# Kernel tuning notes

Measured on AMD Instinct MI355X. Metric: run time of the kernel, lower is better.

## Reference

```python
import jax, jax.numpy as jnp
import numpy as np


def _lstm_layer(x, Wih, Whh, bih, bhh):
    # x: [M, T, D]; Wih: [4H, D]; Whh: [4H, H]; torch gate order i, f, g, o
    M, T, D = x.shape
    H = Whh.shape[1]
    xg = jnp.einsum('mtd,gd->mtg', x, Wih) + bih + bhh  # [M, T, 4H]

    def step(carry, xg_t):
        h, c = carry
        g = xg_t + h @ Whh.T
        i, f, gg, o = jnp.split(g, 4, axis=-1)
        c = jax.nn.sigmoid(f) * c + jax.nn.sigmoid(i) * jnp.tanh(gg)
        h = jax.nn.sigmoid(o) * jnp.tanh(c)
        return (h, c), h

    h0 = jnp.zeros((M, H), x.dtype)
    (_, _), hs = jax.lax.scan(step, (h0, h0), jnp.swapaxes(xg, 0, 1))
    return jnp.swapaxes(hs, 0, 1)  # [M, T, H]


def setup_inputs() -> dict:
    key = jax.random.key(0)
    ks = jax.random.split(key, 16)
    B, T, N = 16, 64, 512
    GH, LH, OUT = 64, 64, 1
    s = 0.1
    inp = {
        'X': jax.random.normal(ks[0], (B, T, N), jnp.float32),
        'adj': jax.random.uniform(ks[1], (N, N), jnp.float32),
        'gcn1_W': jax.random.normal(ks[2], (GH, 1), jnp.float32) * s,
        'gcn1_b': jax.random.normal(ks[3], (GH,), jnp.float32) * s,
        'gcn2_W': jax.random.normal(ks[4], (GH, GH), jnp.float32) * s,
        'gcn2_b': jax.random.normal(ks[5], (GH,), jnp.float32) * s,
        'Wih0': jax.random.normal(ks[6], (4 * LH, GH), jnp.float32) * s,
        'Whh0': jax.random.normal(ks[7], (4 * LH, LH), jnp.float32) * s,
        'bih0': jax.random.normal(ks[8], (4 * LH,), jnp.float32) * s,
        'bhh0': jax.random.normal(ks[9], (4 * LH,), jnp.float32) * s,
        'Wih1': jax.random.normal(ks[10], (4 * LH, LH), jnp.float32) * s,
        'Whh1': jax.random.normal(ks[11], (4 * LH, LH), jnp.float32) * s,
        'bih1': jax.random.normal(ks[12], (4 * LH,), jnp.float32) * s,
        'bhh1': jax.random.normal(ks[13], (4 * LH,), jnp.float32) * s,
        'fc_W': jax.random.normal(ks[14], (OUT, LH), jnp.float32) * s,
        'fc_b': jax.random.normal(ks[15], (OUT,), jnp.float32) * s,
    }
    return inp


def reference(X, adj, gcn1_W, gcn1_b, gcn2_W, gcn2_b,
              Wih0, Whh0, bih0, bhh0, Wih1, Whh1, bih1, bhh1,
              fc_W, fc_b):
    B, T, N = X.shape
    x = X[..., None]  # [B, T, N, 1]
    # GCN layer 1: bmm(A, X) then linear + relu, vectorized over all timesteps
    h = jnp.einsum('nm,btmd->btnd', adj, x)
    h = jax.nn.relu(jnp.einsum('btnd,gd->btng', h, gcn1_W) + gcn1_b)
    # GCN layer 2
    h = jnp.einsum('nm,btmg->btng', adj, h)
    h = jax.nn.relu(jnp.einsum('btng,hg->btnh', h, gcn2_W) + gcn2_b)
    # Per-node LSTM == one batched LSTM over B*N sequences (shared weights)
    GH = h.shape[-1]
    seqs = jnp.transpose(h, (0, 2, 1, 3)).reshape(B * N, T, GH)  # [B*N, T, GH]
    y = _lstm_layer(seqs, Wih0, Whh0, bih0, bhh0)
    y = _lstm_layer(y, Wih1, Whh1, bih1, bhh1)
    last = y[:, -1, :].reshape(B, N, -1)  # [B, N, LH]
    out = jnp.einsum('bnh,oh->bno', last, fc_W) + fc_b  # [B, N, 1]
    return out
```

## Files before the change

### kernel.cpp

```cpp
#include <hip/hip_runtime.h>
#include <hip/hip_bf16.h>

#define Bb 16
#define Tt 64
#define Nn 512
#define BT (Bb*Tt)
#define LH 64
#define Mseq (Bb*Nn)

typedef short  bf16x8 __attribute__((ext_vector_type(8)));
typedef float  f32x16 __attribute__((ext_vector_type(16)));

__device__ __forceinline__ unsigned short f2bf(float f) {
    unsigned int u = __float_as_uint(f);
    return (unsigned short)((u + 0x7FFFu + ((u >> 16) & 1u)) >> 16);
}
__device__ __forceinline__ float bf2f(unsigned short b) {
    return __uint_as_float(((unsigned int)b) << 16);
}
__device__ __forceinline__ void split8(const float* v, bf16x8& hi, bf16x8& lo) {
#pragma unroll
    for (int i = 0; i < 8; ++i) {
        unsigned short h = f2bf(v[i]);
        hi[i] = (short)h;
        lo[i] = (short)f2bf(v[i] - bf2f(h));
    }
}
__device__ __forceinline__ float sigf(float x)  { return 1.f / (1.f + __expf(-x)); }
__device__ __forceinline__ float tanhfast(float x) { return 2.f / (1.f + __expf(-2.f * x)) - 1.f; }

__global__ __launch_bounds__(256) void sgemm_kernel(
    const float* __restrict__ X, const float* __restrict__ adj,
    float* __restrict__ S)
{
    __shared__ __align__(16) float Xs[64 * 68];
    __shared__ __align__(16) float As[64 * 68];
    const int tid = threadIdx.x;
    const int nb  = blockIdx.x * 64;
    const int bt0 = blockIdx.y * 64;

    const int lr  = tid >> 4;
    const int lc4 = (tid & 15) * 4;
    const int r0  = 4 * (tid >> 4);
    const int c0  = 4 * (tid & 15);

    float acc[4][4] = {};

    for (int kc = 0; kc < 8; ++kc) {
        __syncthreads();
#pragma unroll
        for (int s = 0; s < 64; s += 16) {
            *(float4*)&Xs[(lr + s) * 68 + lc4] =
                *(const float4*)&X[(size_t)(bt0 + lr + s) * Nn + kc * 64 + lc4];
            *(float4*)&As[(lr + s) * 68 + lc4] =
                *(const float4*)&adj[(size_t)(nb + lr + s) * Nn + kc * 64 + lc4];
        }
        __syncthreads();
#pragma unroll 4
        for (int k4 = 0; k4 < 64; k4 += 4) {
            float4 x4[4], a4[4];
#pragma unroll
            for (int i = 0; i < 4; ++i) x4[i] = *(float4*)&Xs[(r0 + i) * 68 + k4];
#pragma unroll
            for (int j = 0; j < 4; ++j) a4[j] = *(float4*)&As[(c0 + j) * 68 + k4];
#pragma unroll
            for (int i = 0; i < 4; ++i)
#pragma unroll
                for (int j = 0; j < 4; ++j)
                    acc[i][j] += x4[i].x * a4[j].x + x4[i].y * a4[j].y +
                                 x4[i].z * a4[j].z + x4[i].w * a4[j].w;
        }
    }
#pragma unroll
    for (int i = 0; i < 4; ++i) {
        float4 v = make_float4(acc[i][0], acc[i][1], acc[i][2], acc[i][3]);
        *(float4*)&S[(size_t)(bt0 + r0 + i) * Nn + nb + c0] = v;
    }
}

__global__ __launch_bounds__(256) void adjpack_kernel(
    const float* __restrict__ adj, short* __restrict__ Phi, short* __restrict__ Plo)
{
    const int id   = blockIdx.x * 256 + threadIdx.x;
    const int lane = id & 63;
    const int ks   = (id >> 6) & 3;
    const int sub  = (id >> 8) & 1;
    const int mc   = (id >> 9) & 7;
    const int nt   = (id >> 12) & 7;
    const int row  = nt * 64 + sub * 32 + (lane & 31);

    float v[8];
#pragma unroll
    for (int e = 0; e < 8; ++e) {
        int kk = ((lane >> 5) << 3) + e;
        int ml = ((ks >> 1) << 5) + (kk & 3) + ((kk >> 2) << 3) + ((ks & 1) << 2);
        v[e] = adj[(size_t)row * Nn + mc * 64 + ml];
    }
    bf16x8 hi, lo;
    split8(v, hi, lo);
    *(bf16x8*)&Phi[(size_t)id * 8] = hi;
    *(bf16x8*)&Plo[(size_t)id * 8] = lo;
}

__global__ __launch_bounds__(256) void gcnz_kernel(
    const float* __restrict__ S,
    const short* __restrict__ Phi, const short* __restrict__ Plo,
    const float* __restrict__ w1g, const float* __restrict__ b1g,
    const float* __restrict__ W2, const float* __restrict__ b2g,
    unsigned* __restrict__ outbuf)
{
    __shared__ __align__(16) short zhi[16384];
    __shared__ __align__(16) short zlo[16384];

    const int tid = threadIdx.x;
    const int l   = tid & 63;
    const int w   = tid >> 6;
    const int l31 = l & 31;
    const int lh  = l >> 5;
    const int bt  = blockIdx.x >> 1;
    const int hh  = blockIdx.x & 1;

    bf16x8 w2H[4], w2L[4];
#pragma unroll
    for (int ks = 0; ks < 4; ++ks) {
        int g0 = ks * 16 + lh * 8;
        float v[8];
        *(float4*)&v[0] = *(const float4*)&W2[(size_t)(hh * 32 + l31) * 64 + g0];
        *(float4*)&v[4] = *(const float4*)&W2[(size_t)(hh * 32 + l31) * 64 + g0 + 4];
        split8(v, w2H[ks], w2L[ks]);
    }

#pragma unroll
    for (int mcp = 0; mcp < 2; ++mcp) {
        const int mc = w * 2 + mcp;
#pragma unroll
        for (int msub = 0; msub < 2; ++msub) {
            float s = S[(size_t)bt * Nn + mc * 64 + msub * 32 + l31];
            f32x16 a;
#pragma unroll
            for (int r = 0; r < 16; ++r) a[r] = 0.f;
#pragma unroll
            for (int ks = 0; ks < 4; ++ks) {
                int g0 = ks * 16 + lh * 8;
                float4 wa = *(const float4*)&w1g[g0];
                float4 wb = *(const float4*)&w1g[g0 + 4];
                float4 ba = *(const float4*)&b1g[g0];
                float4 bb = *(const float4*)&b1g[g0 + 4];
                float hv[8];
                hv[0] = fmaxf(s * wa.x + ba.x, 0.f); hv[1] = fmaxf(s * wa.y + ba.y, 0.f);
                hv[2] = fmaxf(s * wa.z + ba.z, 0.f); hv[3] = fmaxf(s * wa.w + ba.w, 0.f);
                hv[4] = fmaxf(s * wb.x + bb.x, 0.f); hv[5] = fmaxf(s * wb.y + bb.y, 0.f);
                hv[6] = fmaxf(s * wb.z + bb.z, 0.f); hv[7] = fmaxf(s * wb.w + bb.w, 0.f);
                bf16x8 h1h, h1l;
                split8(hv, h1h, h1l);
                a = __builtin_amdgcn_mfma_f32_32x32x16_bf16(h1h, w2H[ks], a, 0, 0, 0);
                a = __builtin_amdgcn_mfma_f32_32x32x16_bf16(h1h, w2L[ks], a, 0, 0, 0);
                a = __builtin_amdgcn_mfma_f32_32x32x16_bf16(h1l, w2H[ks], a, 0, 0, 0);
            }
            const int ks_st = msub * 2 + lh;
#pragma unroll
            for (int half = 0; half < 2; ++half) {
                bf16x8 sh, sl;
#pragma unroll
                for (int e = 0; e < 8; ++e) {
                    float v = a[half * 8 + e];
                    unsigned short h = f2bf(v);
                    sh[e] = (short)h;
                    sl[e] = (short)f2bf(v - bf2f(h));
                }
                unsigned off = (unsigned)((mc * 4 + ks_st) * 1024 + (half * 32 + l31) * 16);
                *(bf16x8*)((char*)zhi + off) = sh;
                *(bf16x8*)((char*)zlo + off) = sl;
            }
        }
    }
    __syncthreads();

    const int b = bt >> 6, t = bt & 63;
    const float b2v = b2g[hh * 32 + l31];
#pragma unroll
    for (int nt2 = 0; nt2 < 2; ++nt2) {
        const int nt = w * 2 + nt2;
#pragma unroll
        for (int nsub = 0; nsub < 2; ++nsub) {
            f32x16 a;
#pragma unroll
            for (int r = 0; r < 16; ++r) a[r] = b2v;
            for (int mc = 0; mc < 8; ++mc) {
#pragma unroll
                for (int ks = 0; ks < 4; ++ks) {
                    size_t fo = ((((size_t)(nt * 8 + mc) * 2 + nsub) * 4 + ks) * 64 + l) * 8;
                    bf16x8 ah = *(const bf16x8*)&Phi[fo];
                    bf16x8 al = *(const bf16x8*)&Plo[fo];
                    unsigned zo = (unsigned)((mc * 4 + ks) * 1024 + l * 16);
                    bf16x8 bh = *(bf16x8*)((char*)zhi + zo);
                    bf16x8 bl = *(bf16x8*)((char*)zlo + zo);
                    a = __builtin_amdgcn_mfma_f32_32x32x16_bf16(ah, bh, a, 0, 0, 0);
                    a = __builtin_amdgcn_mfma_f32_32x32x16_bf16(ah, bl, a, 0, 0, 0);
                    a = __builtin_amdgcn_mfma_f32_32x32x16_bf16(al, bh, a, 0, 0, 0);
                }
            }
            const int h = hh * 32 + l31;
#pragma unroll
            for (int r = 0; r < 16; ++r) {
                int n = nt * 64 + nsub * 32 + (r & 3) + 8 * (r >> 2) + 4 * lh;
                float v = fmaxf(a[r], 0.f);
                unsigned short hb = f2bf(v);
                unsigned short lb = f2bf(v - bf2f(hb));
                outbuf[((size_t)(b * Nn + n) * Tt + t) * 64 + h] =
                    ((unsigned)hb << 16) | (unsigned)lb;
            }
        }
    }
}

#define FRS 1072
template <bool LAST>
__global__ __launch_bounds__(512) void lstm_kernel(
    const unsigned* __restrict__ xin, unsigned* __restrict__ yout,
    const float* __restrict__ Wih, const float* __restrict__ Whh,
    const float* __restrict__ bih, const float* __restrict__ bhh,
    const float* __restrict__ fcW, const float* __restrict__ fcb,
    float* __restrict__ out)
{
    __shared__ __align__(16) char xh_[4 * FRS];
    __shared__ __align__(16) char xl_[4 * FRS];
    __shared__ __align__(16) char hh_[4 * FRS];
    __shared__ __align__(16) char hl_[4 * FRS];
    __shared__ float fcp[32 * 17];

    const int tid = threadIdx.x;
    const int l   = tid & 63;
    const int w   = tid >> 6;
    const int l31 = l & 31;
    const int lh1 = l >> 5;
    const int s0  = blockIdx.x * 32;

    bf16x8 wiH[4], wiL[4], whH[4], whL[4];
    {
        const int jg = ((l31 >> 3) << 6) + w * 8 + (l31 & 7);
#pragma unroll
        for (int ks = 0; ks < 4; ++ks) {
            int k0 = ks * 16 + lh1 * 8;
            float v[8];
            *(float4*)&v[0] = *(const float4*)&Wih[(size_t)jg * 64 + k0];
            *(float4*)&v[4] = *(const float4*)&Wih[(size_t)jg * 64 + k0 + 4];
            split8(v, wiH[ks], wiL[ks]);
            *(float4*)&v[0] = *(const float4*)&Whh[(size_t)jg * 64 + k0];
            *(float4*)&v[4] = *(const float4*)&Whh[(size_t)jg * 64 + k0 + 4];
            split8(v, whH[ks], whL[ks]);
        }
    }
    float bias_r[16];
#pragma unroll
    for (int r = 0; r < 16; ++r) {
        int j = ((r >> 2) << 6) + w * 8 + (r & 3) + 4 * lh1;
        bias_r[r] = bih[j] + bhh[j];
    }
    float fw[4];
    if constexpr (LAST) {
#pragma unroll
        for (int i = 0; i < 4; ++i) fw[i] = fcW[w * 8 + 4 * lh1 + i];
    }

    for (int i = tid; i < 4 * FRS / 4; i += 512) {
        ((int*)hh_)[i] = 0;
        ((int*)hl_)[i] = 0;
    }

    const int sm = tid >> 4;
    const int sk = (tid & 15) * 4;
    const unsigned stb = (unsigned)((sk >> 4) * FRS + ((((sk >> 3) & 1) << 5) + sm) * 16 + (sk & 7) * 2);
    const unsigned hwb = (unsigned)((w >> 1) * FRS + (((w & 1) << 5) + l31) * 16 + lh1 * 8);

    float cst[4] = {0.f, 0.f, 0.f, 0.f};
    short4 hph = {0, 0, 0, 0}, hpl = {0, 0, 0, 0};
    float hfin[4];

    uint4 xp = *(const uint4*)&xin[((size_t)(s0 + sm) * Tt + 0) * 64 + sk];

    for (int t = 0; t < Tt; ++t) {
        short4 sh, sl;
        sh.x = (short)(xp.x >> 16); sl.x = (short)(xp.x & 0xffff);
        sh.y = (short)(xp.y >> 16); sl.y = (short)(xp.y & 0xffff);
        sh.z = (short)(xp.z >> 16); sl.z = (short)(xp.z & 0xffff);
        sh.w = (short)(xp.w >> 16); sl.w = (short)(xp.w & 0xffff);
        *(short4*)(xh_ + stb) = sh;
        *(short4*)(xl_ + stb) = sl;
        if (t > 0) {
            *(short4*)(hh_ + hwb) = hph;
            *(short4*)(hl_ + hwb) = hpl;
        }
        {
            int tn = (t < Tt - 1) ? t + 1 : t;
            xp = *(const uint4*)&xin[((size_t)(s0 + sm) * Tt + tn) * 64 + sk];
        }
        __syncthreads();

        f32x16 a1, a2;
#pragma unroll
        for (int r = 0; r < 16; ++r) { a1[r] = 0.f; a2[r] = 0.f; }
#pragma unroll
        for (int ks = 0; ks < 4; ++ks) {
            bf16x8 xh = *(bf16x8*)(xh_ + ks * FRS + l * 16);
            bf16x8 xl = *(bf16x8*)(xl_ + ks * FRS + l * 16);
            a1 = __builtin_amdgcn_mfma_f32_32x32x16_bf16(wiH[ks], xh, a1, 0, 0, 0);
            a1 = __builtin_amdgcn_mfma_f32_32x32x16_bf16(wiL[ks], xh, a1, 0, 0, 0);
            a1 = __builtin_amdgcn_mfma_f32_32x32x16_bf16(wiH[ks], xl, a1, 0, 0, 0);
            bf16x8 hh = *(bf16x8*)(hh_ + ks * FRS + l * 16);
            bf16x8 hl = *(bf16x8*)(hl_ + ks * FRS + l * 16);
            a2 = __builtin_amdgcn_mfma_f32_32x32x16_bf16(whH[ks], hh, a2, 0, 0, 0);
            a2 = __builtin_amdgcn_mfma_f32_32x32x16_bf16(whL[ks], hh, a2, 0, 0, 0);
            a2 = __builtin_amdgcn_mfma_f32_32x32x16_bf16(whH[ks], hl, a2, 0, 0, 0);
        }

        unsigned yq[4];
#pragma unroll
        for (int ui = 0; ui < 4; ++ui) {
            float gi = a1[ui]      + a2[ui]      + bias_r[ui];
            float gf = a1[4 + ui]  + a2[4 + ui]  + bias_r[4 + ui];
            float gg = a1[8 + ui]  + a2[8 + ui]  + bias_r[8 + ui];
            float go = a1[12 + ui] + a2[12 + ui] + bias_r[12 + ui];
            float c  = sigf(gf) * cst[ui] + sigf(gi) * tanhfast(gg);
            float hv = sigf(go) * tanhfast(c);
            cst[ui] = c;
            unsigned short hb = f2bf(hv);
            unsigned short lb = f2bf(hv - bf2f(hb));
            ((short*)&hph)[ui] = (short)hb;
            ((short*)&hpl)[ui] = (short)lb;
            if constexpr (!LAST) {
                yq[ui] = ((unsigned)hb << 16) | (unsigned)lb;
            } else {
                if (t == Tt - 1) hfin[ui] = hv;
            }
        }
        if constexpr (!LAST) {
            *(uint4*)&yout[((size_t)(s0 + l31) * Tt + t) * 64 + w * 8 + 4 * lh1] =
                make_uint4(yq[0], yq[1], yq[2], yq[3]);
        }
        __syncthreads();
    }

    if constexpr (LAST) {
        float part = hfin[0] * fw[0] + hfin[1] * fw[1] + hfin[2] * fw[2] + hfin[3] * fw[3];
        fcp[l31 * 17 + w * 2 + lh1] = part;
        __syncthreads();
        if (tid < 32) {
            float s = fcb[0];
#pragma unroll
            for (int i = 0; i < 16; ++i) s += fcp[tid * 17 + i];
            out[s0 + tid] = s;
        }
    }
}

extern "C" void kernel_launch(void* const* d_in, const int* in_sizes, int n_in,
                              void* d_out, int out_size, void* d_ws, size_t ws_size,
                              hipStream_t stream) {
    const float* X      = (const float*)d_in[0];
    const float* adj    = (const float*)d_in[1];
    const float* gcn1_W = (const float*)d_in[2];
    const float* gcn1_b = (const float*)d_in[3];
    const float* gcn2_W = (const float*)d_in[4];
    const float* gcn2_b = (const float*)d_in[5];
    const float* Wih0   = (const float*)d_in[6];
    const float* Whh0   = (const float*)d_in[7];
    const float* bih0   = (const float*)d_in[8];
    const float* bhh0   = (const float*)d_in[9];
    const float* Wih1   = (const float*)d_in[10];
    const float* Whh1   = (const float*)d_in[11];
    const float* bih1   = (const float*)d_in[12];
    const float* bhh1   = (const float*)d_in[13];
    const float* fc_W   = (const float*)d_in[14];
    const float* fc_b   = (const float*)d_in[15];

    char* base = (char*)d_ws;
    float*    S      = (float*)base;
    unsigned* buf0   = (unsigned*)(base + (size_t)BT * Nn * 4);
    short*    adjPhi = (short*)(base + (size_t)BT * Nn * 4 + (size_t)Mseq * Tt * LH * 4);
    short*    adjPlo = adjPhi + 32768 * 8;

    sgemm_kernel<<<dim3(Nn / 64, BT / 64), 256, 0, stream>>>(X, adj, S);
    adjpack_kernel<<<128, 256, 0, stream>>>(adj, adjPhi, adjPlo);
    gcnz_kernel<<<2048, 256, 0, stream>>>(
        S, adjPhi, adjPlo, gcn1_W, gcn1_b, gcn2_W, gcn2_b, buf0);
    lstm_kernel<false><<<Mseq / 32, 512, 0, stream>>>(
        buf0, buf0, Wih0, Whh0, bih0, bhh0, nullptr, nullptr, nullptr);
    lstm_kernel<true><<<Mseq / 32, 512, 0, stream>>>(
        buf0, nullptr, Wih1, Whh1, bih1, bhh1, fc_W, fc_b, (float*)d_out);
}
```

Before: 644.3 us.

## Fuse GCN layer-2 bmm with per-timestep weight matmul and split LSTM accumulators

The GCN kernel no longer stages the full Z=h1·W2 for a timestep in shared memory. Each block now handles four timesteps (one per wave) and one 64-node tile, computing Z chunks in registers and feeding them straight into the adjacency bmm, with the adjacency fragments repacked to match. This removes the 64KB LDS buffer and its barrier and adds an occupancy hint, but every wave now reloads adjacency fragments from global memory and recomputes the split-bf16 conversion. In the LSTM kernel, the MFMA chain uses two independent accumulator pairs to shorten dependency chains, and the x/h staging moves after the compute with an extra barrier.

```diff
diff --git a/kernel.cpp b/kernel.cpp
--- a/kernel.cpp
+++ b/kernel.cpp
@@ -81,142 +81,168 @@
 __global__ __launch_bounds__(256) void adjpack_kernel(
     const float* __restrict__ adj, short* __restrict__ Phi, short* __restrict__ Plo)
 {
-    const int id   = blockIdx.x * 256 + threadIdx.x;
-    const int lane = id & 63;
-    const int ks   = (id >> 6) & 3;
-    const int sub  = (id >> 8) & 1;
-    const int mc   = (id >> 9) & 7;
-    const int nt   = (id >> 12) & 7;
-    const int row  = nt * 64 + sub * 32 + (lane & 31);
+    const int g    = blockIdx.x * 256 + threadIdx.x;
+    const int lane = g & 63;
+    const int ks   = (g >> 6) & 1;
+    const int ns   = (g >> 7) & 1;
+    const int ms   = (g >> 8) & 15;
+    const int nt   = (g >> 12) & 7;
+    const int n    = nt * 64 + ns * 32 + (lane & 31);
+    const int lh   = lane >> 5;
 
     float v[8];
 #pragma unroll
     for (int e = 0; e < 8; ++e) {
-        int kk = ((lane >> 5) << 3) + e;
-        int ml = ((ks >> 1) << 5) + (kk & 3) + ((kk >> 2) << 3) + ((ks & 1) << 2);
-        v[e] = adj[(size_t)row * Nn + mc * 64 + ml];
+        int pi = ks * 16 + lh * 4 + (e & 3) + 8 * (e >> 2);
+        v[e] = adj[(size_t)n * Nn + ms * 32 + pi];
     }
     bf16x8 hi, lo;
     split8(v, hi, lo);
-    *(bf16x8*)&Phi[(size_t)id * 8] = hi;
-    *(bf16x8*)&Plo[(size_t)id * 8] = lo;
-}
-
-__global__ __launch_bounds__(256) void gcnz_kernel(
+    *(bf16x8*)&Phi[(size_t)g * 8] = hi;
+    *(bf16x8*)&Plo[(size_t)g * 8] = lo;
+}
+
+__device__ __forceinline__ void bmm_step(
+    const f32x16& az, const short* __restrict__ Phi, const short* __restrict__ Plo,
+    size_t abase, int l, f32x16& acc_ns0, f32x16& acc_ns1)
+{
+    bf16x8 zH[2], zL[2];
+#pragma unroll
+    for (int kb = 0; kb < 2; ++kb) {
+#pragma unroll
+        for (int e = 0; e < 8; ++e) {
+            float v = az[kb * 8 + e];
+            unsigned short hb = f2bf(v);
+            zH[kb][e] = (short)hb;
+            zL[kb][e] = (short)f2bf(v - bf2f(hb));
+        }
+    }
+#pragma unroll
+    for (int ns = 0; ns < 2; ++ns) {
+#pragma unroll
+        for (int kb = 0; kb < 2; ++kb) {
+            size_t fo = abase + (size_t)((ns * 2 + kb) * 64 + l) * 8;
+            bf16x8 ah = *(const bf16x8*)&Phi[fo];
+            bf16x8 al = *(const bf16x8*)&Plo[fo];
+            if (ns == 0) {
+                acc_ns0 = __builtin_amdgcn_mfma_f32_32x32x16_bf16(ah, zH[kb], acc_ns0, 0, 0, 0);
+                acc_ns0 = __builtin_amdgcn_mfma_f32_32x32x16_bf16(ah, zL[kb], acc_ns0, 0, 0, 0);
+                acc_ns0 = __builtin_amdgcn_mfma_f32_32x32x16_bf16(al, zH[kb], acc_ns0, 0, 0, 0);
+            } else {
+                acc_ns1 = __builtin_amdgcn_mfma_f32_32x32x16_bf16(ah, zH[kb], acc_ns1, 0, 0, 0);
+                acc_ns1 = __builtin_amdgcn_mfma_f32_32x32x16_bf16(ah, zL[kb], acc_ns1, 0, 0, 0);
+                acc_ns1 = __builtin_amdgcn_mfma_f32_32x32x16_bf16(al, zH[kb], acc_ns1, 0, 0, 0);
+            }
+        }
+    }
+}
+
+__global__ __launch_bounds__(256, 2) void gcnz_kernel(
     const float* __restrict__ S,
     const short* __restrict__ Phi, const short* __restrict__ Plo,
     const float* __restrict__ w1g, const float* __restrict__ b1g,
     const float* __restrict__ W2, const float* __restrict__ b2g,
     unsigned* __restrict__ outbuf)
 {
-    __shared__ __align__(16) short zhi[16384];
-    __shared__ __align__(16) short zlo[16384];
-
     const int tid = threadIdx.x;
     const int l   = tid & 63;
     const int w   = tid >> 6;
     const int l31 = l & 31;
     const int lh  = l >> 5;
-    const int bt  = blockIdx.x >> 1;
-    const int hh  = blockIdx.x & 1;
-
-    bf16x8 w2H[4], w2L[4];
-#pragma unroll
-    for (int ks = 0; ks < 4; ++ks) {
-        int g0 = ks * 16 + lh * 8;
-        float v[8];
-        *(float4*)&v[0] = *(const float4*)&W2[(size_t)(hh * 32 + l31) * 64 + g0];
-        *(float4*)&v[4] = *(const float4*)&W2[(size_t)(hh * 32 + l31) * 64 + g0 + 4];
-        split8(v, w2H[ks], w2L[ks]);
-    }
-
-#pragma unroll
-    for (int mcp = 0; mcp < 2; ++mcp) {
-        const int mc = w * 2 + mcp;
-#pragma unroll
-        for (int msub = 0; msub < 2; ++msub) {
-            float s = S[(size_t)bt * Nn + mc * 64 + msub * 32 + l31];
-            f32x16 a;
-#pragma unroll
-            for (int r = 0; r < 16; ++r) a[r] = 0.f;
-#pragma unroll
-            for (int ks = 0; ks < 4; ++ks) {
-                int g0 = ks * 16 + lh * 8;
+    const int btg = blockIdx.x >> 3;
+    const int nt  = blockIdx.x & 7;
+    const int bt  = btg * 4 + w;
+
+    bf16x8 w2H[2][4], w2L[2][4];
+#pragma unroll
+    for (int hh = 0; hh < 2; ++hh)
+#pragma unroll
+        for (int kg = 0; kg < 4; ++kg) {
+            float v[8];
+            const float* p = &W2[(size_t)(hh * 32 + l31) * 64 + kg * 16 + lh * 8];
+            *(float4*)&v[0] = *(const float4*)&p[0];
+            *(float4*)&v[4] = *(const float4*)&p[4];
+            split8(v, w2H[hh][kg], w2L[hh][kg]);
+        }
+
+    f32x16 o00, o01, o10, o11;
+    {
+        float b20 = b2g[l31], b21 = b2g[32 + l31];
+#pragma unroll
+        for (int r = 0; r < 16; ++r) { o00[r] = b20; o01[r] = b21; o10[r] = b20; o11[r] = b21; }
+    }
+
+    const float* Srow = &S[(size_t)bt * Nn];
+
+    for (int mc = 0; mc < 8; ++mc) {
+#pragma unroll
+        for (int ms = 0; ms < 2; ++ms) {
+            const float sv = Srow[mc * 64 + ms * 32 + l31];
+            f32x16 az0, az1;
+#pragma unroll
+            for (int r = 0; r < 16; ++r) { az0[r] = 0.f; az1[r] = 0.f; }
+#pragma unroll
+            for (int kg = 0; kg < 4; ++kg) {
+                int g0 = kg * 16 + lh * 8;
                 float4 wa = *(const float4*)&w1g[g0];
                 float4 wb = *(const float4*)&w1g[g0 + 4];
                 float4 ba = *(const float4*)&b1g[g0];
                 float4 bb = *(const float4*)&b1g[g0 + 4];
                 float hv[8];
-                hv[0] = fmaxf(s * wa.x + ba.x, 0.f); hv[1] = fmaxf(s * wa.y + ba.y, 0.f);
-                hv[2] = fmaxf(s * wa.z + ba.z, 0.f); hv[3] = fmaxf(s * wa.w + ba.w, 0.f);
-                hv[4] = fmaxf(s * wb.x + bb.x, 0.f); hv[5] = fmaxf(s * wb.y + bb.y, 0.f);
-                hv[6] = fmaxf(s * wb.z + bb.z, 0.f); hv[7] = fmaxf(s * wb.w + bb.w, 0.f);
+                hv[0] = fmaxf(sv * wa.x + ba.x, 0.f); hv[1] = fmaxf(sv * wa.y + ba.y, 0.f);
+                hv[2] = fmaxf(sv * wa.z + ba.z, 0.f); hv[3] = fmaxf(sv * wa.w + ba.w, 0.f);
+                hv[4] = fmaxf(sv * wb.x + bb.x, 0.f); hv[5] = fmaxf(sv * wb.y + bb.y, 0.f);
+                hv[6] = fmaxf(sv * wb.z + bb.z, 0.f); hv[7] = fmaxf(sv * wb.w + bb.w, 0.f);
                 bf16x8 h1h, h1l;
                 split8(hv, h1h, h1l);
-                a = __builtin_amdgcn_mfma_f32_32x32x16_bf16(h1h, w2H[ks], a, 0, 0, 0);
-                a = __builtin_amdgcn_mfma_f32_32x32x16_bf16(h1h, w2L[ks], a, 0, 0, 0);
-                a = __builtin_amdgcn_mfma_f32_32x32x16_bf16(h1l, w2H[ks], a, 0, 0, 0);
+                az0 = __builtin_amdgcn_mfma_f32_32x32x16_bf16(h1h, w2H[0][kg], az0, 0, 0, 0);
+                az0 = __builtin_amdgcn_mfma_f32_32x32x16_bf16(h1h, w2L[0][kg], az0, 0, 0, 0);
+                az0 = __builtin_amdgcn_mfma_f32_32x32x16_bf16(h1l, w2H[0][kg], az0, 0, 0, 0);
+                az1 = __builtin_amdgcn_mfma_f32_32x32x16_bf16(h1h, w2H[1][kg], az1, 0, 0, 0);
+                az1 = __builtin_amdgcn_mfma_f32_32x32x16_bf16(h1h, w2L[1][kg], az1, 0, 0, 0);
+                az1 = __builtin_amdgcn_mfma_f32_32x32x16_bf16(h1l, w2H[1][kg], az1, 0, 0, 0);
             }
-            const int ks_st = msub * 2 + lh;
-#pragma unroll
-            for (int half = 0; half < 2; ++half) {
-                bf16x8 sh, sl;
-#pragma unroll
-                for (int e = 0; e < 8; ++e) {
-                    float v = a[half * 8 + e];
-                    unsigned short h = f2bf(v);
-                    sh[e] = (short)h;
-                    sl[e] = (short)f2bf(v - bf2f(h));
-                }
-                unsigned off = (unsigned)((mc * 4 + ks_st) * 1024 + (half * 32 + l31) * 16);
-                *(bf16x8*)((char*)zhi + off) = sh;
-                *(bf16x8*)((char*)zlo + off) = sl;
-            }
-        }
-    }
-    __syncthreads();
+            const size_t abase = (size_t)(nt * 16 + mc * 2 + ms) * 2048;
+            bmm_step(az0, Phi, Plo, abase, l, o00, o10);
+            bmm_step(az1, Phi, Plo, abase, l, o01, o11);
+        }
+    }
 
     const int b = bt >> 6, t = bt & 63;
-    const float b2v = b2g[hh * 32 + l31];
-#pragma unroll
-    for (int nt2 = 0; nt2 < 2; ++nt2) {
-        const int nt = w * 2 + nt2;
-#pragma unroll
-        for (int nsub = 0; nsub < 2; ++nsub) {
-            f32x16 a;
-#pragma unroll
-            for (int r = 0; r < 16; ++r) a[r] = b2v;
-            for (int mc = 0; mc < 8; ++mc) {
-#pragma unroll
-                for (int ks = 0; ks < 4; ++ks) {
-                    size_t fo = ((((size_t)(nt * 8 + mc) * 2 + nsub) * 4 + ks) * 64 + l) * 8;
-                    bf16x8 ah = *(const bf16x8*)&Phi[fo];
-                    bf16x8 al = *(const bf16x8*)&Plo[fo];
-                    unsigned zo = (unsigned)((mc * 4 + ks) * 1024 + l * 16);
-                    bf16x8 bh = *(bf16x8*)((char*)zhi + zo);
-                    bf16x8 bl = *(bf16x8*)((char*)zlo + zo);
-                    a = __builtin_amdgcn_mfma_f32_32x32x16_bf16(ah, bh, a, 0, 0, 0);
-                    a = __builtin_amdgcn_mfma_f32_32x32x16_bf16(ah, bl, a, 0, 0, 0);
-                    a = __builtin_amdgcn_mfma_f32_32x32x16_bf16(al, bh, a, 0, 0, 0);
-                }
-            }
-            const int h = hh * 32 + l31;
-#pragma unroll
-            for (int r = 0; r < 16; ++r) {
-                int n = nt * 64 + nsub * 32 + (r & 3) + 8 * (r >> 2) + 4 * lh;
-                float v = fmaxf(a[r], 0.f);
-                unsigned short hb = f2bf(v);
-                unsigned short lb = f2bf(v - bf2f(hb));
-                outbuf[((size_t)(b * Nn + n) * Tt + t) * 64 + h] =
-                    ((unsigned)hb << 16) | (unsigned)lb;
-            }
-        }
-    }
+#define STORE_ACC(ACC, NS, HH)                                                  \
+    {                                                                           \
+        _Pragma("unroll")                                                       \
+        for (int r = 0; r < 16; ++r) {                                          \
+            int n = nt * 64 + (NS) * 32 + (r & 3) + 8 * (r >> 2) + 4 * lh;      \
+            int h = (HH) * 32 + l31;                                            \
+            float v = fmaxf(ACC[r], 0.f);                                       \
+            unsigned short hb = f2bf(v);                                        \
+            unsigned short lb = f2bf(v - bf2f(hb));                             \
+            outbuf[((size_t)(b * Nn + n) * Tt + t) * 64 + h] =                  \
+                ((unsigned)hb << 16) | (unsigned)lb;                            \
+        }                                                                       \
+    }
+    STORE_ACC(o00, 0, 0)
+    STORE_ACC(o01, 0, 1)
+    STORE_ACC(o10, 1, 0)
+    STORE_ACC(o11, 1, 1)
+#undef STORE_ACC
 }
 
 #define FRS 1072
+
+__device__ __forceinline__ void stage_x(uint4 xp, unsigned stb, char* xh_, char* xl_) {
+    short4 sh, sl;
+    sh.x = (short)(xp.x >> 16); sl.x = (short)(xp.x & 0xffff);
+    sh.y = (short)(xp.y >> 16); sl.y = (short)(xp.y & 0xffff);
+    sh.z = (short)(xp.z >> 16); sl.z = (short)(xp.z & 0xffff);
+    sh.w = (short)(xp.w >> 16); sl.w = (short)(xp.w & 0xffff);
+    *(short4*)(xh_ + stb) = sh;
+    *(short4*)(xl_ + stb) = sl;
+}
+
 template <bool LAST>
-__global__ __launch_bounds__(512) void lstm_kernel(
+__global__ __launch_bounds__(512, 2) void lstm_kernel(
     const unsigned* __restrict__ xin, unsigned* __restrict__ yout,
     const float* __restrict__ Wih, const float* __restrict__ Whh,
     const float* __restrict__ bih, const float* __restrict__ bhh,
@@ -274,60 +300,57 @@
     const unsigned hwb = (unsigned)((w >> 1) * FRS + (((w & 1) << 5) + l31) * 16 + lh1 * 8);
 
     float cst[4] = {0.f, 0.f, 0.f, 0.f};
-    short4 hph = {0, 0, 0, 0}, hpl = {0, 0, 0, 0};
-    float hfin[4];
-
-    uint4 xp = *(const uint4*)&xin[((size_t)(s0 + sm) * Tt + 0) * 64 + sk];
+    float hfin[4] = {0.f, 0.f, 0.f, 0.f};
+
+    {
+        uint4 xp = *(const uint4*)&xin[((size_t)(s0 + sm) * Tt + 0) * 64 + sk];
+        stage_x(xp, stb, xh_, xl_);
+    }
+    __syncthreads();
 
     for (int t = 0; t < Tt; ++t) {
-        short4 sh, sl;
-        sh.x = (short)(xp.x >> 16); sl.x = (short)(xp.x & 0xffff);
-        sh.y = (short)(xp.y >> 16); sl.y = (short)(xp.y & 0xffff);
-        sh.z = (short)(xp.z >> 16); sl.z = (short)(xp.z & 0xffff);
-        sh.w = (short)(xp.w >> 16); sl.w = (short)(xp.w & 0xffff);
-        *(short4*)(xh_ + stb) = sh;
-        *(short4*)(xl_ + stb) = sl;
-        if (t > 0) {
-            *(short4*)(hh_ + hwb) = hph;
-            *(short4*)(hl_ + hwb) = hpl;
-        }
-        {
-            int tn = (t < Tt - 1) ? t + 1 : t;
-            xp = *(const uint4*)&xin[((size_t)(s0 + sm) * Tt + tn) * 64 + sk];
-        }
-        __syncthreads();
-
-        f32x16 a1, a2;
-#pragma unroll
-        for (int r = 0; r < 16; ++r) { a1[r] = 0.f; a2[r] = 0.f; }
-#pragma unroll
-        for (int ks = 0; ks < 4; ++ks) {
-            bf16x8 xh = *(bf16x8*)(xh_ + ks * FRS + l * 16);
-            bf16x8 xl = *(bf16x8*)(xl_ + ks * FRS + l * 16);
-            a1 = __builtin_amdgcn_mfma_f32_32x32x16_bf16(wiH[ks], xh, a1, 0, 0, 0);
-            a1 = __builtin_amdgcn_mfma_f32_32x32x16_bf16(wiL[ks], xh, a1, 0, 0, 0);
-            a1 = __builtin_amdgcn_mfma_f32_32x32x16_bf16(wiH[ks], xl, a1, 0, 0, 0);
-            bf16x8 hh = *(bf16x8*)(hh_ + ks * FRS + l * 16);
-            bf16x8 hl = *(bf16x8*)(hl_ + ks * FRS + l * 16);
-            a2 = __builtin_amdgcn_mfma_f32_32x32x16_bf16(whH[ks], hh, a2, 0, 0, 0);
-            a2 = __builtin_amdgcn_mfma_f32_32x32x16_bf16(whL[ks], hh, a2, 0, 0, 0);
-            a2 = __builtin_amdgcn_mfma_f32_32x32x16_bf16(whH[ks], hl, a2, 0, 0, 0);
-        }
-
+        uint4 xq;
+        if (t < Tt - 1)
+            xq = *(const uint4*)&xin[((size_t)(s0 + sm) * Tt + (t + 1)) * 64 + sk];
+
+        f32x16 p0, p1, q0, q1;
+#pragma unroll
+        for (int r = 0; r < 16; ++r) { p0[r] = 0.f; p1[r] = 0.f; q0[r] = 0.f; q1[r] = 0.f; }
+
+#define LSTEP(KS, PX, QX)                                                        \
+        {                                                                        \
+            bf16x8 xh = *(bf16x8*)(xh_ + (KS) * FRS + l * 16);                   \
+            bf16x8 xl = *(bf16x8*)(xl_ + (KS) * FRS + l * 16);                   \
+            PX = __builtin_amdgcn_mfma_f32_32x32x16_bf16(wiH[KS], xh, PX, 0, 0, 0); \
+            PX = __builtin_amdgcn_mfma_f32_32x32x16_bf16(wiL[KS], xh, PX, 0, 0, 0); \
+            PX = __builtin_amdgcn_mfma_f32_32x32x16_bf16(wiH[KS], xl, PX, 0, 0, 0); \
+            bf16x8 hh = *(bf16x8*)(hh_ + (KS) * FRS + l * 16);                   \
+            bf16x8 hl = *(bf16x8*)(hl_ + (KS) * FRS + l * 16);                   \
+            QX = __builtin_amdgcn_mfma_f32_32x32x16_bf16(whH[KS], hh, QX, 0, 0, 0); \
+            QX = __builtin_amdgcn_mfma_f32_32x32x16_bf16(whL[KS], hh, QX, 0, 0, 0); \
+            QX = __builtin_amdgcn_mfma_f32_32x32x16_bf16(whH[KS], hl, QX, 0, 0, 0); \
+        }
+        LSTEP(0, p0, q0)
+        LSTEP(1, p1, q1)
+        LSTEP(2, p0, q0)
+        LSTEP(3, p1, q1)
+#undef LSTEP
+
+        short4 nh, nl;
         unsigned yq[4];
 #pragma unroll
         for (int ui = 0; ui < 4; ++ui) {
-            float gi = a1[ui]      + a2[ui]      + bias_r[ui];
-            float gf = a1[4 + ui]  + a2[4 + ui]  + bias_r[4 + ui];
-            float gg = a1[8 + ui]  + a2[8 + ui]  + bias_r[8 + ui];
-            float go = a1[12 + ui] + a2[12 + ui] + bias_r[12 + ui];
+            float gi = p0[ui]      + p1[ui]      + q0[ui]      + q1[ui]      + bias_r[ui];
+            float gf = p0[4 + ui]  + p1[4 + ui]  + q0[4 + ui]  + q1[4 + ui]  + bias_r[4 + ui];
+            float gg = p0[8 + ui]  + p1[8 + ui]  + q0[8 + ui]  + q1[8 + ui]  + bias_r[8 + ui];
+            float go = p0[12 + ui] + p1[12 + ui] + q0[12 + ui] + q1[12 + ui] + bias_r[12 + ui];
             float c  = sigf(gf) * cst[ui] + sigf(gi) * tanhfast(gg);
             float hv = sigf(go) * tanhfast(c);
             cst[ui] = c;
             unsigned short hb = f2bf(hv);
             unsigned short lb = f2bf(hv - bf2f(hb));
-            ((short*)&hph)[ui] = (short)hb;
-            ((short*)&hpl)[ui] = (short)lb;
+            ((short*)&nh)[ui] = (short)hb;
+            ((short*)&nl)[ui] = (short)lb;
             if constexpr (!LAST) {
                 yq[ui] = ((unsigned)hb << 16) | (unsigned)lb;
             } else {
@@ -337,6 +360,12 @@
         if constexpr (!LAST) {
             *(uint4*)&yout[((size_t)(s0 + l31) * Tt + t) * 64 + w * 8 + 4 * lh1] =
                 make_uint4(yq[0], yq[1], yq[2], yq[3]);
+        }
+        __syncthreads();
+        if (t < Tt - 1) {
+            stage_x(xq, stb, xh_, xl_);
+            *(short4*)(hh_ + hwb) = nh;
+            *(short4*)(hl_ + hwb) = nl;
         }
         __syncthreads();
     }
```

Result: no change. 640.4 us (-0.6%).
